# Optimization experiments

Hardware: AMD Instinct MI355X
Metric: run time of the kernel (lower is better)

Reference implementation:

```python
import jax, jax.numpy as jnp
import numpy as np

B, L, D, H = 8, 1024, 768, 12
HD = D // H
EPS = 1e-5
R_EPS = 1e-12  # numerical guard for r at coincident positions


def setup_inputs() -> dict:
    key = jax.random.key(0)
    ks = jax.random.split(key, 8)
    x = jax.random.normal(ks[0], (B, L, D), dtype=jnp.float32)
    # 32x32 patch grid coordinates, same for every batch element
    g = jnp.arange(32, dtype=jnp.float32)
    yy, xx = jnp.meshgrid(g, g, indexing='ij')
    pos = jnp.broadcast_to(jnp.stack([yy.ravel(), xx.ravel()], axis=-1), (B, L, 2))
    w_norm = jnp.ones((D,), dtype=jnp.float32)
    w_in = 0.02 * jax.random.normal(ks[1], (3 * D, D), dtype=jnp.float32)
    b_in = jnp.zeros((3 * D,), dtype=jnp.float32)
    w_out = 0.02 * jax.random.normal(ks[2], (D, D), dtype=jnp.float32)
    b_out = jnp.zeros((D,), dtype=jnp.float32)
    # bias params [H, 6] = (o, c, w, p, delta, m) per init_bias_params
    o = jnp.zeros((H,), dtype=jnp.float32)
    c = 1.0 + 0.3 * jax.random.uniform(ks[3], (H,), dtype=jnp.float32)
    w = jnp.ones((H,), dtype=jnp.float32)
    p = jnp.zeros((H,), dtype=jnp.float32)
    delta = jax.random.normal(ks[4], (H,), dtype=jnp.float32)
    m = jnp.ones((H,), dtype=jnp.float32)
    bias_params = jnp.stack([o, c, w, p, delta, m], axis=-1)
    return {"x": x, "pos": pos, "w_norm": w_norm, "w_in": w_in, "b_in": b_in,
            "w_out": w_out, "b_out": b_out, "bias_params": bias_params}


def _bias_grid(pos, bias_params):
    # pos: [B, L, 2] -> bias: [B, H, L, L]
    o, c, w, p, delta, m = [bias_params[:, i].reshape(1, H, 1, 1) for i in range(6)]
    dist = pos[:, :, None, :] - pos[:, None, :, :]          # [B, Lq, Lk, 2]
    theta = jnp.arctan2(dist[..., 1], dist[..., 0])[:, None]  # [B, 1, Lq, Lk]
    r = jnp.sqrt(jnp.sum(dist * dist, axis=-1) + R_EPS)[:, None]
    term1 = jax.nn.relu(r - o) ** jnp.abs(c)
    term2 = 1.0 - jnp.abs(jnp.tanh(delta)) * (jnp.cos((theta - p) * w * 0.5) ** 2) ** jnp.abs(m)
    return term1 * term2


def reference(x, pos, w_norm, w_in, b_in, w_out, b_out, bias_params):
    bias = _bias_grid(pos, bias_params)                      # [B, H, L, L]
    # RMSNorm
    xn = x * jax.lax.rsqrt(jnp.mean(x * x, axis=-1, keepdims=True) + EPS) * w_norm
    qkv = xn @ w_in.T + b_in                                 # [B, L, 3D]
    q, k, v = jnp.split(qkv, 3, axis=-1)
    def heads(t):
        return t.reshape(B, L, H, HD).transpose(0, 2, 1, 3)  # [B, H, L, HD]
    q, k, v = heads(q), heads(k), heads(v)
    scores = jnp.einsum('bhqd,bhkd->bhqk', q, k) / jnp.sqrt(jnp.float32(HD)) + bias
    attn = jax.nn.softmax(scores, axis=-1)
    o = jnp.einsum('bhqk,bhkd->bhqd', attn, v)
    o = o.transpose(0, 2, 1, 3).reshape(B, L, D)
    return o @ w_out.T + b_out
```

## Files before the change

### kernel.cpp

```cpp
#include <hip/hip_runtime.h>

#define BB 8
#define LL 1024
#define DD 768
#define HH 12
#define HD 64

typedef short s16x8 __attribute__((ext_vector_type(8)));
typedef float f32x4 __attribute__((ext_vector_type(4)));
typedef unsigned int u32x4 __attribute__((ext_vector_type(4)));

static __device__ __forceinline__ unsigned short f2bf(float f){
  unsigned int u = __builtin_bit_cast(unsigned int, f);
  u = (u + 0x7FFFu + ((u >> 16) & 1u)) >> 16;
  return (unsigned short)u;
}

static __device__ __forceinline__ unsigned int cvtpk_bf(float a, float b){
  unsigned int r;
  asm("v_cvt_pk_bf16_f32 %0, %1, %2" : "=v"(r) : "v"(a), "v"(b));
  return r;
}

static __device__ __forceinline__ void swap32(unsigned int& a, unsigned int& b){
  asm("v_permlane32_swap_b32 %0, %1" : "+v"(a), "+v"(b));
}
static __device__ __forceinline__ void swap16(unsigned int& a, unsigned int& b){
  asm("v_permlane16_swap_b32 %0, %1" : "+v"(a), "+v"(b));
}

static __device__ __forceinline__ f32x4 mfma16(s16x8 a, s16x8 b, f32x4 c){
  return __builtin_amdgcn_mfma_f32_16x16x32_bf16(a, b, c, 0, 0, 0);
}

static __device__ __forceinline__ void gld_lds16(const void* g, void* l){
  __builtin_amdgcn_global_load_lds(
      (const __attribute__((address_space(1))) void*)g,
      (__attribute__((address_space(3))) void*)l, 16, 0, 0);
}

__global__ void cvt_kernel(const float* __restrict__ src, unsigned short* __restrict__ dst, int n4){
  int i = blockIdx.x*256 + threadIdx.x;
  if (i < n4){
    float4 v = ((const float4*)src)[i];
    ushort4 o;
    o.x = f2bf(v.x); o.y = f2bf(v.y); o.z = f2bf(v.z); o.w = f2bf(v.w);
    ((ushort4*)dst)[i] = o;
  }
}

__global__ void bias_table_kernel(const float* __restrict__ bp, float* __restrict__ table){
  int idx = blockIdx.x*256 + threadIdx.x;
  if (idx >= HH*3969) return;
  int hh = idx/3969, rem = idx - hh*3969;
  int dy = rem/63 - 31, dx = rem%63 - 31;
  float o  = bp[hh*6+0], c = bp[hh*6+1], w = bp[hh*6+2];
  float p  = bp[hh*6+3], dl = bp[hh*6+4], m = bp[hh*6+5];
  float theta = atan2f((float)dx, (float)dy);
  float r = sqrtf((float)(dy*dy + dx*dx) + 1e-12f);
  float t1 = powf(fmaxf(r - o, 0.0f), fabsf(c));
  float co = cosf((theta - p)*w*0.5f);
  float t2 = 1.0f - fabsf(tanhf(dl))*powf(co*co, fabsf(m));
  table[idx] = t1*t2*1.44269504f;
}

__global__ __launch_bounds__(64) void bmax_kernel(const float* __restrict__ table,
                                                  float* __restrict__ bmax){
  int qy = blockIdx.x, h = blockIdx.y;
  __shared__ float m1[63];
  int t = threadIdx.x;
  const float* tb = table + h*3969;
  if (t < 63){
    float m = -3.0e38f;
    #pragma unroll 4
    for (int row = qy; row < qy + 32; row++) m = fmaxf(m, tb[row*63 + t]);
    m1[t] = m;
  }
  __syncthreads();
  if (t < 32){
    float m = -3.0e38f;
    #pragma unroll 4
    for (int c = t; c < t + 32; c++) m = fmaxf(m, m1[c]);
    bmax[(h*32 + qy)*32 + t] = m;
  }
}

__global__ __launch_bounds__(256) void rmsnorm_kernel(const float* __restrict__ x,
                                                      const float* __restrict__ wn,
                                                      unsigned short* __restrict__ xn){
  int row = blockIdx.x, t = threadIdx.x;
  const float* xr = x + (size_t)row*DD;
  float v0 = xr[t], v1 = xr[t+256], v2 = xr[t+512];
  float ss = v0*v0 + v1*v1 + v2*v2;
  #pragma unroll
  for (int m = 1; m < 64; m <<= 1) ss += __shfl_xor(ss, m, 64);
  __shared__ float red[4];
  if ((t & 63) == 0) red[t >> 6] = ss;
  __syncthreads();
  float tot = red[0] + red[1] + red[2] + red[3];
  float sc = rsqrtf(tot*(1.0f/DD) + 1e-5f);
  unsigned short* xo = xn + (size_t)row*DD;
  xo[t]     = f2bf(v0*sc*wn[t]);
  xo[t+256] = f2bf(v1*sc*wn[t+256]);
  xo[t+512] = f2bf(v2*sc*wn[t+512]);
}

static __device__ __forceinline__ void storeC(float* p, float v){ *p = v; }
static __device__ __forceinline__ void storeC(unsigned short* p, float v){ *p = f2bf(v); }

template<int MODE, int TN, typename OutT>
__global__ __launch_bounds__(256) void gemm_bt_kernel(const unsigned short* __restrict__ A,
                                                      const unsigned short* __restrict__ B,
                                                      const float* __restrict__ bias,
                                                      OutT* __restrict__ C,
                                                      unsigned short* __restrict__ qp,
                                                      unsigned short* __restrict__ kp,
                                                      unsigned short* __restrict__ vp,
                                                      int M, int N, int K){
  constexpr int NT = TN/32;
  __shared__ __align__(16) unsigned short As[3][128*32];
  __shared__ __align__(16) unsigned short Bs[3][TN*32];
  int tid = threadIdx.x;
  int w = tid >> 6, lane = tid & 63, quad = lane >> 4, col = lane & 15;
  int wm = (w >> 1)*64, wn = (w & 1)*(TN/2);
  int bm = blockIdx.x*128, bn = blockIdx.y*TN;

  int srow = lane >> 2;
  int schunk = (lane & 3)*8;
  const unsigned short* ga0 = A + (size_t)(bm + w*32 + srow)*K + schunk;
  const unsigned short* ga1 = ga0 + (size_t)16*K;
  const unsigned short* gb0 = B + (size_t)(bn + w*(TN/4) + srow)*K + schunk;
  const unsigned short* gb1 = gb0 + (size_t)16*K;

  auto stage = [&](int t, int b){
    int kk = t*32;
    gld_lds16(ga0 + kk, As[b] + (w*32)*32);
    gld_lds16(ga1 + kk, As[b] + (w*32 + 16)*32);
    gld_lds16(gb0 + kk, Bs[b] + (w*(TN/4))*32);
    if (TN == 128) gld_lds16(gb1 + kk, Bs[b] + (w*32 + 16)*32);
  };

  f32x4 acc[4][NT];
  #pragma unroll
  for (int mt = 0; mt < 4; mt++)
    #pragma unroll
    for (int nt = 0; nt < NT; nt++) acc[mt][nt] = (f32x4){0.f,0.f,0.f,0.f};

  stage(0, 0);
  stage(1, 1);

  int KT = K >> 5;
  int buf = 0, nbuf = 2;
  for (int t = 0; t < KT; t++){
    if (t < KT - 1){
      if (TN == 128) asm volatile("s_waitcnt vmcnt(4)" ::: "memory");
      else           asm volatile("s_waitcnt vmcnt(3)" ::: "memory");
    } else {
      asm volatile("s_waitcnt vmcnt(0)" ::: "memory");
    }
    __builtin_amdgcn_s_barrier();
    asm volatile("" ::: "memory");
    if (t + 2 < KT) stage(t + 2, nbuf);
    s16x8 af[4], bfr[NT];
    #pragma unroll
    for (int mt = 0; mt < 4; mt++)
      af[mt] = *(const s16x8*)&As[buf][(wm + mt*16 + col)*32 + quad*8];
    #pragma unroll
    for (int nt = 0; nt < NT; nt++)
      bfr[nt] = *(const s16x8*)&Bs[buf][(wn + nt*16 + col)*32 + quad*8];
    #pragma unroll
    for (int mt = 0; mt < 4; mt++)
      #pragma unroll
      for (int nt = 0; nt < NT; nt++)
        acc[mt][nt] = mfma16(af[mt], bfr[nt], acc[mt][nt]);
    buf  = (buf  == 2) ? 0 : buf  + 1;
    nbuf = (nbuf == 2) ? 0 : nbuf + 1;
  }

  #pragma unroll
  for (int mt = 0; mt < 4; mt++)
    #pragma unroll
    for (int nt = 0; nt < NT; nt++){
      int cl = bn + wn + nt*16 + col;
      float bv = bias[cl];
      #pragma unroll
      for (int r = 0; r < 4; r++){
        int rw = bm + wm + mt*16 + quad*4 + r;
        float v = acc[mt][nt][r] + bv;
        if (MODE == 0){
          storeC(&C[(size_t)rw*N + cl], v);
        } else {
          int part = cl >= 1536 ? 2 : (cl >= 768 ? 1 : 0);
          int hd = cl - part*768;
          int h = hd >> 6, d = hd & 63;
          int bb = rw >> 10, l = rw & 1023;
          size_t base = (((size_t)bb*HH + h)*LL + l)*64;
          unsigned short v16 = f2bf(v);
          if (part == 0)      qp[base + d] = v16;
          else if (part == 1) kp[base + ((((d>>3) ^ (l&7)) << 3) | (d & 7))] = v16;
          else                vp[base + d] = v16;
        }
      }
    }
}

__global__ __launch_bounds__(256) void vtrans_kernel(const unsigned short* __restrict__ vp,
                                                     unsigned short* __restrict__ vt2){
  int jt = blockIdx.x, bh = blockIdx.y;
  __shared__ unsigned short tile[32][68];
  int t = threadIdx.x;
  const unsigned short* src = vp + ((size_t)bh*LL + jt*32)*64;
  #pragma unroll
  for (int e = 0; e < 8; e++){
    int lin = t + 256*e;
    tile[lin >> 6][lin & 63] = src[lin];
  }
  __syncthreads();
  unsigned short* dst = vt2 + ((size_t)bh*32 + jt)*2048;
  #pragma unroll
  for (int e = 0; e < 8; e++){
    int lin = t + 256*e;
    dst[lin] = tile[lin & 31][lin >> 5];
  }
}

__global__ __launch_bounds__(256) void attn_kernel(const unsigned short* __restrict__ qp,
                                                   const unsigned short* __restrict__ kp,
                                                   const unsigned short* __restrict__ vt2,
                                                   const float* __restrict__ table,
                                                   const float* __restrict__ bmax,
                                                   const float* __restrict__ pos,
                                                   unsigned short* __restrict__ o_out){
  int i = blockIdx.x;
  int bh = (i >> 6)*8 + (i & 7);
  int qt = (i >> 3) & 7;
  int b = bh/HH, h = bh - b*HH;
  int tid = threadIdx.x, w = tid >> 6, lane = tid & 63, quad = lane >> 4, col = lane & 15;
  __shared__ float tl[3969];
  __shared__ int ky63[32];
  __shared__ __align__(16) unsigned short Ks[3][2048];
  __shared__ __align__(16) unsigned short Vs[3][2048];

  const unsigned short* kgp = kp  + (size_t)bh*65536;
  const unsigned short* vgp = vt2 + (size_t)bh*65536;
  int soff = w*512 + lane*8;

  gld_lds16(kgp + soff,        &Ks[0][w*512]);
  gld_lds16(vgp + soff,        &Vs[0][w*512]);
  gld_lds16(kgp + 2048 + soff, &Ks[1][w*512]);
  gld_lds16(vgp + 2048 + soff, &Vs[1][w*512]);

  for (int j = tid; j < 3969; j += 256) tl[j] = table[h*3969 + j];
  const float* pb = pos + (size_t)b*2048;
  if (tid < 32) ky63[tid] = 63*__float2int_rn(pb[tid*64]);
  __syncthreads();

  int qw = qt*128 + w*32;
  const unsigned short* qpb = qp + (size_t)bh*65536;
  s16x8 qa[2][2];
  int cq[2];
  f32x4 zb[2];
  #pragma unroll
  for (int g = 0; g < 2; g++){
    int q = qw + g*16 + col;
    size_t qo = (size_t)q*64 + quad*8;
    qa[g][0] = *(const s16x8*)(qpb + qo);
    qa[g][1] = *(const s16x8*)(qpb + qo + 32);
    int qy = __float2int_rn(pb[q*2]);
    int qx = __float2int_rn(pb[q*2 + 1]);
    cq[g] = qy*63 + qx + 1984 - quad*4;
    float neg = -5.5451774445f * bmax[(h*32 + qy)*32 + qx];
    zb[g] = (f32x4){neg, neg, neg, neg};
  }

  s16x8 ones;
  #pragma unroll
  for (int e = 0; e < 8; e++) ones[e] = (short)0x3F80;

  int sw = col & 7;
  int a_k0 = col*128 + ((quad    ) ^ sw)*16;
  int a_k1 = col*128 + ((quad + 4) ^ sw)*16;
  int a_k2 = a_k0 + 2048;
  int a_k3 = a_k1 + 2048;
  int a_v  = col*64 + quad*16;

  f32x4 o[2][4];
  f32x4 l_acc[2];
  #pragma unroll
  for (int g = 0; g < 2; g++){
    #pragma unroll
    for (int nt = 0; nt < 4; nt++) o[g][nt] = (f32x4){0.f,0.f,0.f,0.f};
    l_acc[g] = (f32x4){0.f,0.f,0.f,0.f};
  }

  int buf = 0, nbuf = 2;
  for (int t = 0; t < 32; t++){
    if (t < 31) asm volatile("s_waitcnt vmcnt(2)" ::: "memory");
    else        asm volatile("s_waitcnt vmcnt(0)" ::: "memory");
    __builtin_amdgcn_s_barrier();
    asm volatile("" ::: "memory");
    if (t + 2 < 32){
      gld_lds16(kgp + (t+2)*2048 + soff, &Ks[nbuf][w*512]);
      gld_lds16(vgp + (t+2)*2048 + soff, &Vs[nbuf][w*512]);
    }
    const char* kb = (const char*)Ks[buf];
    const char* vb = (const char*)Vs[buf];
    s16x8 k0 = *(const s16x8*)(kb + a_k0);
    s16x8 k1 = *(const s16x8*)(kb + a_k1);
    s16x8 k2 = *(const s16x8*)(kb + a_k2);
    s16x8 k3 = *(const s16x8*)(kb + a_k3);
    s16x8 v0 = *(const s16x8*)(vb + a_v);
    s16x8 v1 = *(const s16x8*)(vb + a_v + 1024);
    s16x8 v2 = *(const s16x8*)(vb + a_v + 2048);
    s16x8 v3 = *(const s16x8*)(vb + a_v + 3072);
    int kyt = ky63[t];

    __builtin_amdgcn_s_setprio(1);
    #pragma unroll
    for (int g = 0; g < 2; g++){
      f32x4 s_lo = mfma16(k0, qa[g][0], zb[g]);  s_lo = mfma16(k1, qa[g][1], s_lo);
      f32x4 s_hi = mfma16(k2, qa[g][0], zb[g]);  s_hi = mfma16(k3, qa[g][1], s_hi);
      int base = cq[g] - kyt;
      float pl[4], ph[4];
      #pragma unroll
      for (int r = 0; r < 4; r++){
        pl[r] = exp2f(__builtin_fmaf(s_lo[r], 0.18033688f, tl[base - r]));
        ph[r] = exp2f(__builtin_fmaf(s_hi[r], 0.18033688f, tl[base - r - 16]));
      }
      unsigned int wA = cvtpk_bf(pl[0], pl[1]);
      unsigned int wB = cvtpk_bf(pl[2], pl[3]);
      unsigned int wC = cvtpk_bf(ph[0], ph[1]);
      unsigned int wD = cvtpk_bf(ph[2], ph[3]);
      swap32(wA, wC);  swap32(wB, wD);
      swap16(wA, wC);  swap16(wB, wD);
      u32x4 pv4; pv4.x = wA; pv4.y = wB; pv4.z = wC; pv4.w = wD;
      s16x8 pf = __builtin_bit_cast(s16x8, pv4);
      l_acc[g] = mfma16(ones, pf, l_acc[g]);
      o[g][0] = mfma16(v0, pf, o[g][0]);
      o[g][1] = mfma16(v1, pf, o[g][1]);
      o[g][2] = mfma16(v2, pf, o[g][2]);
      o[g][3] = mfma16(v3, pf, o[g][3]);
    }
    __builtin_amdgcn_s_setprio(0);
    buf  = (buf  == 2) ? 0 : buf  + 1;
    nbuf = (nbuf == 2) ? 0 : nbuf + 1;
  }

  #pragma unroll
  for (int g = 0; g < 2; g++){
    float inv = 1.0f / l_acc[g][0];
    int q = qw + g*16 + col;
    unsigned short* orow = o_out + (size_t)(b*LL + q)*DD + h*64;
    #pragma unroll
    for (int nt = 0; nt < 4; nt++){
      uint2 pkd;
      pkd.x = cvtpk_bf(o[g][nt][0]*inv, o[g][nt][1]*inv);
      pkd.y = cvtpk_bf(o[g][nt][2]*inv, o[g][nt][3]*inv);
      *(uint2*)&orow[nt*16 + quad*4] = pkd;
    }
  }
}

extern "C" void kernel_launch(void* const* d_in, const int* in_sizes, int n_in,
                              void* d_out, int out_size, void* d_ws, size_t ws_size,
                              hipStream_t stream){
  const float* x      = (const float*)d_in[0];
  const float* pos    = (const float*)d_in[1];
  const float* w_norm = (const float*)d_in[2];
  const float* w_in   = (const float*)d_in[3];
  const float* b_in   = (const float*)d_in[4];
  const float* w_out  = (const float*)d_in[5];
  const float* b_out  = (const float*)d_in[6];
  const float* bp     = (const float*)d_in[7];

  char* ws = (char*)d_ws;
  unsigned short* xn    = (unsigned short*)(ws);
  unsigned short* winb  = (unsigned short*)(ws + 12582912);
  unsigned short* woutb = (unsigned short*)(ws + 16121856);
  unsigned short* qpb   = (unsigned short*)(ws + 17301504);
  unsigned short* kpb   = (unsigned short*)(ws + 29884416);
  unsigned short* vpb   = (unsigned short*)(ws + 42467328);
  unsigned short* vt2b  = (unsigned short*)(ws + 55050240);
  float*          table = (float*)        (ws + 67633152);
  unsigned short* ob    = (unsigned short*)(ws + 67823664);
  float*          bmaxp = (float*)        (ws);

  cvt_kernel<<<dim3((2304*768/4)/256), dim3(256), 0, stream>>>(w_in, winb, 2304*768/4);
  cvt_kernel<<<dim3((768*768/4)/256), dim3(256), 0, stream>>>(w_out, woutb, 768*768/4);
  bias_table_kernel<<<dim3((HH*3969 + 255)/256), dim3(256), 0, stream>>>(bp, table);
  rmsnorm_kernel<<<dim3(BB*LL), dim3(256), 0, stream>>>(x, w_norm, xn);
  gemm_bt_kernel<1, 128, unsigned short><<<dim3(64, 18), dim3(256), 0, stream>>>(
      xn, winb, b_in, (unsigned short*)nullptr, qpb, kpb, vpb, BB*LL, 3*DD, DD);
  bmax_kernel<<<dim3(32, HH), dim3(64), 0, stream>>>(table, bmaxp);
  vtrans_kernel<<<dim3(32, BB*HH), dim3(256), 0, stream>>>(vpb, vt2b);
  attn_kernel<<<dim3(768), dim3(256), 0, stream>>>(qpb, kpb, vt2b, table, bmaxp, pos, ob);
  gemm_bt_kernel<0, 64, float><<<dim3(64, 12), dim3(256), 0, stream>>>(
      ob, woutb, b_out, (float*)d_out, nullptr, nullptr, nullptr, BB*LL, DD, DD);
}
```

Measured before the change: 244.1 us.

## Load K/V tiles straight into registers and stage QKV epilogue via LDS

```diff
diff --git a/kernel.cpp b/kernel.cpp
--- a/kernel.cpp
+++ b/kernel.cpp
@@ -27,6 +27,14 @@
 }
 static __device__ __forceinline__ void swap16(unsigned int& a, unsigned int& b){
   asm("v_permlane16_swap_b32 %0, %1" : "+v"(a), "+v"(b));
+}
+
+static __device__ __forceinline__ float hexp2(float x){
+#if __has_builtin(__builtin_amdgcn_exp2f)
+  return __builtin_amdgcn_exp2f(x);
+#else
+  return exp2f(x);
+#endif
 }
 
 static __device__ __forceinline__ f32x4 mfma16(s16x8 a, s16x8 b, f32x4 c){
@@ -118,8 +126,10 @@
                                                       unsigned short* __restrict__ vp,
                                                       int M, int N, int K){
   constexpr int NT = TN/32;
-  __shared__ __align__(16) unsigned short As[3][128*32];
-  __shared__ __align__(16) unsigned short Bs[3][TN*32];
+  constexpr int SMEM_BYTES = 192*(128 + TN);
+  __shared__ __align__(16) char smem[SMEM_BYTES];
+  unsigned short* As = (unsigned short*)smem;
+  unsigned short* Bs = (unsigned short*)(smem + 3*128*32*2);
   int tid = threadIdx.x;
   int w = tid >> 6, lane = tid & 63, quad = lane >> 4, col = lane & 15;
   int wm = (w >> 1)*64, wn = (w & 1)*(TN/2);
@@ -132,12 +142,12 @@
   const unsigned short* gb0 = B + (size_t)(bn + w*(TN/4) + srow)*K + schunk;
   const unsigned short* gb1 = gb0 + (size_t)16*K;
 
-  auto stage = [&](int t, int b){
+  auto stage = [&](int t, int bi){
     int kk = t*32;
-    gld_lds16(ga0 + kk, As[b] + (w*32)*32);
-    gld_lds16(ga1 + kk, As[b] + (w*32 + 16)*32);
-    gld_lds16(gb0 + kk, Bs[b] + (w*(TN/4))*32);
-    if (TN == 128) gld_lds16(gb1 + kk, Bs[b] + (w*32 + 16)*32);
+    gld_lds16(ga0 + kk, As + bi*4096 + (w*32)*32);
+    gld_lds16(ga1 + kk, As + bi*4096 + (w*32 + 16)*32);
+    gld_lds16(gb0 + kk, Bs + bi*(TN*32) + (w*(TN/4))*32);
+    if (TN == 128) gld_lds16(gb1 + kk, Bs + bi*(TN*32) + (w*32 + 16)*32);
   };
 
   f32x4 acc[4][NT];
@@ -164,10 +174,10 @@
     s16x8 af[4], bfr[NT];
     #pragma unroll
     for (int mt = 0; mt < 4; mt++)
-      af[mt] = *(const s16x8*)&As[buf][(wm + mt*16 + col)*32 + quad*8];
+      af[mt] = *(const s16x8*)&As[buf*4096 + (wm + mt*16 + col)*32 + quad*8];
     #pragma unroll
     for (int nt = 0; nt < NT; nt++)
-      bfr[nt] = *(const s16x8*)&Bs[buf][(wn + nt*16 + col)*32 + quad*8];
+      bfr[nt] = *(const s16x8*)&Bs[buf*(TN*32) + (wn + nt*16 + col)*32 + quad*8];
     #pragma unroll
     for (int mt = 0; mt < 4; mt++)
       #pragma unroll
@@ -177,31 +187,52 @@
     nbuf = (nbuf == 2) ? 0 : nbuf + 1;
   }
 
-  #pragma unroll
-  for (int mt = 0; mt < 4; mt++)
-    #pragma unroll
-    for (int nt = 0; nt < NT; nt++){
-      int cl = bn + wn + nt*16 + col;
-      float bv = bias[cl];
+  if (MODE == 1){
+    __syncthreads();
+    unsigned short* Ct = (unsigned short*)smem;
+    #pragma unroll
+    for (int mt = 0; mt < 4; mt++)
       #pragma unroll
-      for (int r = 0; r < 4; r++){
-        int rw = bm + wm + mt*16 + quad*4 + r;
-        float v = acc[mt][nt][r] + bv;
-        if (MODE == 0){
-          storeC(&C[(size_t)rw*N + cl], v);
-        } else {
-          int part = cl >= 1536 ? 2 : (cl >= 768 ? 1 : 0);
-          int hd = cl - part*768;
-          int h = hd >> 6, d = hd & 63;
-          int bb = rw >> 10, l = rw & 1023;
-          size_t base = (((size_t)bb*HH + h)*LL + l)*64;
-          unsigned short v16 = f2bf(v);
-          if (part == 0)      qp[base + d] = v16;
-          else if (part == 1) kp[base + ((((d>>3) ^ (l&7)) << 3) | (d & 7))] = v16;
-          else                vp[base + d] = v16;
+      for (int nt = 0; nt < NT; nt++){
+        int cc = wn + nt*16 + col;
+        float bv = bias[bn + cc];
+        #pragma unroll
+        for (int r = 0; r < 4; r++){
+          int row = wm + mt*16 + quad*4 + r;
+          Ct[row*136 + cc] = f2bf(acc[mt][nt][r] + bv);
         }
       }
+    __syncthreads();
+    #pragma unroll
+    for (int e = 0; e < 8; e++){
+      int id = e*256 + tid;
+      int row = id >> 4, ch = id & 15;
+      s16x8 val = *(const s16x8*)&Ct[row*136 + ch*8];
+      int rw = bm + row;
+      int cl0 = bn + ch*8;
+      int part = cl0 >= 1536 ? 2 : (cl0 >= 768 ? 1 : 0);
+      int hd = cl0 - part*768;
+      int hh2 = hd >> 6, d0 = hd & 63;
+      int bb = rw >> 10, l = rw & 1023;
+      size_t base = (((size_t)bb*HH + hh2)*LL + l)*64;
+      if (part == 0)      *(s16x8*)(qp + base + d0) = val;
+      else if (part == 1) *(s16x8*)(kp + base + (((d0>>3) ^ (l&7)) << 3)) = val;
+      else                *(s16x8*)(vp + base + d0) = val;
     }
+  } else {
+    #pragma unroll
+    for (int mt = 0; mt < 4; mt++)
+      #pragma unroll
+      for (int nt = 0; nt < NT; nt++){
+        int cl = bn + wn + nt*16 + col;
+        float bv = bias[cl];
+        #pragma unroll
+        for (int r = 0; r < 4; r++){
+          int rw = bm + wm + mt*16 + quad*4 + r;
+          storeC(&C[(size_t)rw*N + cl], acc[mt][nt][r] + bv);
+        }
+      }
+  }
 }
 
 __global__ __launch_bounds__(256) void vtrans_kernel(const unsigned short* __restrict__ vp,
@@ -237,23 +268,33 @@
   int b = bh/HH, h = bh - b*HH;
   int tid = threadIdx.x, w = tid >> 6, lane = tid & 63, quad = lane >> 4, col = lane & 15;
   __shared__ float tl[3969];
-  __shared__ int ky63[32];
-  __shared__ __align__(16) unsigned short Ks[3][2048];
-  __shared__ __align__(16) unsigned short Vs[3][2048];
 
   const unsigned short* kgp = kp  + (size_t)bh*65536;
   const unsigned short* vgp = vt2 + (size_t)bh*65536;
-  int soff = w*512 + lane*8;
-
-  gld_lds16(kgp + soff,        &Ks[0][w*512]);
-  gld_lds16(vgp + soff,        &Vs[0][w*512]);
-  gld_lds16(kgp + 2048 + soff, &Ks[1][w*512]);
-  gld_lds16(vgp + 2048 + soff, &Vs[1][w*512]);
+
+  int sw = col & 7;
+  int k_r0 = col*64 + ((quad ^ sw) << 3);
+  int k_r1 = col*64 + (((quad + 4) ^ sw) << 3);
+  int v_r  = col*32 + quad*8;
+
+  s16x8 kA[4], vA[4], kB[4], vB[4];
+  auto issue = [&](int t, s16x8 (&k)[4], s16x8 (&v)[4]){
+    const unsigned short* kt = kgp + t*2048;
+    const unsigned short* vt = vgp + t*2048;
+    k[0] = *(const s16x8*)(kt + k_r0);
+    k[1] = *(const s16x8*)(kt + k_r1);
+    k[2] = *(const s16x8*)(kt + 1024 + k_r0);
+    k[3] = *(const s16x8*)(kt + 1024 + k_r1);
+    v[0] = *(const s16x8*)(vt + v_r);
+    v[1] = *(const s16x8*)(vt + v_r + 512);
+    v[2] = *(const s16x8*)(vt + v_r + 1024);
+    v[3] = *(const s16x8*)(vt + v_r + 1536);
+  };
+  issue(0, kA, vA);
+  issue(1, kB, vB);
 
   for (int j = tid; j < 3969; j += 256) tl[j] = table[h*3969 + j];
   const float* pb = pos + (size_t)b*2048;
-  if (tid < 32) ky63[tid] = 63*__float2int_rn(pb[tid*64]);
-  __syncthreads();
 
   int qw = qt*128 + w*32;
   const unsigned short* qpb = qp + (size_t)bh*65536;
@@ -277,13 +318,6 @@
   #pragma unroll
   for (int e = 0; e < 8; e++) ones[e] = (short)0x3F80;
 
-  int sw = col & 7;
-  int a_k0 = col*128 + ((quad    ) ^ sw)*16;
-  int a_k1 = col*128 + ((quad + 4) ^ sw)*16;
-  int a_k2 = a_k0 + 2048;
-  int a_k3 = a_k1 + 2048;
-  int a_v  = col*64 + quad*16;
-
   f32x4 o[2][4];
   f32x4 l_acc[2];
   #pragma unroll
@@ -293,39 +327,20 @@
     l_acc[g] = (f32x4){0.f,0.f,0.f,0.f};
   }
 
-  int buf = 0, nbuf = 2;
-  for (int t = 0; t < 32; t++){
-    if (t < 31) asm volatile("s_waitcnt vmcnt(2)" ::: "memory");
-    else        asm volatile("s_waitcnt vmcnt(0)" ::: "memory");
-    __builtin_amdgcn_s_barrier();
-    asm volatile("" ::: "memory");
-    if (t + 2 < 32){
-      gld_lds16(kgp + (t+2)*2048 + soff, &Ks[nbuf][w*512]);
-      gld_lds16(vgp + (t+2)*2048 + soff, &Vs[nbuf][w*512]);
-    }
-    const char* kb = (const char*)Ks[buf];
-    const char* vb = (const char*)Vs[buf];
-    s16x8 k0 = *(const s16x8*)(kb + a_k0);
-    s16x8 k1 = *(const s16x8*)(kb + a_k1);
-    s16x8 k2 = *(const s16x8*)(kb + a_k2);
-    s16x8 k3 = *(const s16x8*)(kb + a_k3);
-    s16x8 v0 = *(const s16x8*)(vb + a_v);
-    s16x8 v1 = *(const s16x8*)(vb + a_v + 1024);
-    s16x8 v2 = *(const s16x8*)(vb + a_v + 2048);
-    s16x8 v3 = *(const s16x8*)(vb + a_v + 3072);
-    int kyt = ky63[t];
-
-    __builtin_amdgcn_s_setprio(1);
+  __syncthreads();
+
+  auto step = [&](int t, s16x8 (&k)[4], s16x8 (&v)[4]){
+    int kyt = 63*t;
     #pragma unroll
     for (int g = 0; g < 2; g++){
-      f32x4 s_lo = mfma16(k0, qa[g][0], zb[g]);  s_lo = mfma16(k1, qa[g][1], s_lo);
-      f32x4 s_hi = mfma16(k2, qa[g][0], zb[g]);  s_hi = mfma16(k3, qa[g][1], s_hi);
+      f32x4 s_lo = mfma16(k[0], qa[g][0], zb[g]);  s_lo = mfma16(k[1], qa[g][1], s_lo);
+      f32x4 s_hi = mfma16(k[2], qa[g][0], zb[g]);  s_hi = mfma16(k[3], qa[g][1], s_hi);
       int base = cq[g] - kyt;
       float pl[4], ph[4];
       #pragma unroll
       for (int r = 0; r < 4; r++){
-        pl[r] = exp2f(__builtin_fmaf(s_lo[r], 0.18033688f, tl[base - r]));
-        ph[r] = exp2f(__builtin_fmaf(s_hi[r], 0.18033688f, tl[base - r - 16]));
+        pl[r] = hexp2(__builtin_fmaf(s_lo[r], 0.18033688f, tl[base - r]));
+        ph[r] = hexp2(__builtin_fmaf(s_hi[r], 0.18033688f, tl[base - r - 16]));
       }
       unsigned int wA = cvtpk_bf(pl[0], pl[1]);
       unsigned int wB = cvtpk_bf(pl[2], pl[3]);
@@ -336,14 +351,18 @@
       u32x4 pv4; pv4.x = wA; pv4.y = wB; pv4.z = wC; pv4.w = wD;
       s16x8 pf = __builtin_bit_cast(s16x8, pv4);
       l_acc[g] = mfma16(ones, pf, l_acc[g]);
-      o[g][0] = mfma16(v0, pf, o[g][0]);
-      o[g][1] = mfma16(v1, pf, o[g][1]);
-      o[g][2] = mfma16(v2, pf, o[g][2]);
-      o[g][3] = mfma16(v3, pf, o[g][3]);
+      o[g][0] = mfma16(v[0], pf, o[g][0]);
+      o[g][1] = mfma16(v[1], pf, o[g][1]);
+      o[g][2] = mfma16(v[2], pf, o[g][2]);
+      o[g][3] = mfma16(v[3], pf, o[g][3]);
     }
-    __builtin_amdgcn_s_setprio(0);
-    buf  = (buf  == 2) ? 0 : buf  + 1;
-    nbuf = (nbuf == 2) ? 0 : nbuf + 1;
+  };
+
+  for (int t = 0; t < 32; t += 2){
+    step(t, kA, vA);
+    if (t + 2 < 32) issue(t + 2, kA, vA);
+    step(t + 1, kB, vB);
+    if (t + 3 < 32) issue(t + 3, kB, vB);
   }
 
   #pragma unroll
```

After: 226.0 us. 7.4% less time.
